# Optimization experiments

Measured on AMD Instinct MI355X. Metric: run time of the kernel, lower is better.

The kernel has to match this reference:

```python
import jax, jax.numpy as jnp
import numpy as np

INP, OUP, KSIZE, STRIDE = 256, 256, 3, 1
M, G = 2, 2
INP_GAP = max(16, INP // 16)  # 16
PAD = KSIZE // 2


def setup_inputs() -> dict:
    key = jax.random.key(0)
    k1, k2, k3, k4, k5 = jax.random.split(key, 5)
    B, H, W = 32, 28, 28
    x = jax.random.normal(k1, (B, INP, H, W), dtype=jnp.float32)
    x_gap = jax.random.normal(k2, (B, INP_GAP, 1, 1), dtype=jnp.float32)
    # wn_fc1: Conv2d(INP_GAP, M*OUP, 1, bias=True) -> dense [M*OUP, INP_GAP]
    w1 = jax.random.normal(k3, (M * OUP, INP_GAP), dtype=jnp.float32) * 0.1
    b1 = jax.random.normal(k4, (M * OUP,), dtype=jnp.float32) * 0.1
    # wn_fc2: grouped 1x1 conv, groups = G*OUP, 1 in-channel per group
    # -> weight is effectively a vector of length OUP*INP*KSIZE*KSIZE
    w2 = jax.random.normal(k5, (OUP * INP * KSIZE * KSIZE,), dtype=jnp.float32) * 0.05
    return {"x": x, "x_gap": x_gap, "w1": w1, "b1": b1, "w2": w2}


def reference(x, x_gap, w1, b1, w2):
    B, _, H, W = x.shape
    # fc1 (1x1 conv on [B, INP_GAP, 1, 1]) + sigmoid -> [B, M*OUP]
    h = jax.nn.sigmoid(jnp.einsum('bi,oi->bo', x_gap[:, :, 0, 0], w1) + b1)
    # fc2: groups = G*OUP, one input channel per group, INP*K*K/G outputs per group
    per = INP * KSIZE * KSIZE // G
    # [B, G*OUP, per] -> per-sample kernels [B*OUP, INP, K, K]
    wk = (w2.reshape(G * OUP, per) * h[:, :, None]).reshape(B * OUP, INP, KSIZE, KSIZE)
    # batched dynamic conv via feature_group_count = B
    y = jax.lax.conv_general_dilated(
        x.reshape(1, B * INP, H, W), wk,
        window_strides=(STRIDE, STRIDE),
        padding=[(PAD, PAD), (PAD, PAD)],
        dimension_numbers=('NCHW', 'OIHW', 'NCHW'),
        feature_group_count=B)
    return y.reshape(B, OUP, y.shape[2], y.shape[3])
```

## Files before the change

### kernel.cpp

```cpp
#include <hip/hip_runtime.h>
#include <hip/hip_bf16.h>

typedef __attribute__((ext_vector_type(8))) short bf16x8;
typedef __attribute__((ext_vector_type(4))) short bf16x4;
typedef __attribute__((ext_vector_type(4))) float f32x4;

#define NB 32
#define NO 256

static __device__ __forceinline__ void gld16(const void* g, void* l) {
    __builtin_amdgcn_global_load_lds(
        (const __attribute__((address_space(1))) void*)g,
        (__attribute__((address_space(3))) void*)l, 16, 0, 0);
}

__global__ void prep_kernel(const float* __restrict__ w2, __hip_bfloat16* __restrict__ wrt) {
    int idx = blockIdx.x * 256 + threadIdx.x;
    int kcol = idx & 15;
    int klo = (idx >> 4) & 3;
    int mf = (idx >> 6) & 3;
    int mw = (idx >> 8) & 3;
    int kw2 = (idx >> 10) & 1;
    int s = idx >> 11;
    int tap = s >> 2;
    int ic = s & 3;
    int o = mw * 64 + mf * 16 + kcol;
    int ch = kw2 * 128 + ic * 32 + klo * 8;
    const float* src = w2 + (size_t)o * 2304 + (size_t)ch * 9 + tap;
    union { bf16x8 v; __hip_bfloat16 e[8]; } u;
#pragma unroll
    for (int e = 0; e < 8; ++e) u.e[e] = __float2bfloat16(src[e * 9]);
    *(bf16x8*)((short*)wrt + (size_t)idx * 8) = u.v;
}

#define MM(A_, B_, mf_, nf_) \
    acc[mf_][nf_] = __builtin_amdgcn_mfma_f32_16x16x32_bf16(A_, B_, acc[mf_][nf_], 0, 0, 0);

#define CL_H1(A0, A1, A2, A3, B0, B1, B2, B3)                           \
    __builtin_amdgcn_s_setprio(1);                                      \
    MM(A0, B0, 0, 0) MM(A1, B0, 1, 0) MM(A2, B0, 2, 0) MM(A3, B0, 3, 0) \
    MM(A0, B1, 0, 1) MM(A1, B1, 1, 1) MM(A2, B1, 2, 1) MM(A3, B1, 3, 1) \
    MM(A0, B2, 0, 2) MM(A1, B2, 1, 2) MM(A2, B2, 2, 2) MM(A3, B2, 3, 2) \
    MM(A0, B3, 0, 3) MM(A1, B3, 1, 3) MM(A2, B3, 2, 3) MM(A3, B3, 3, 3) \
    __builtin_amdgcn_s_setprio(0);
#define CL_H2(A0, A1, A2, A3, B4, B5, B6)                               \
    __builtin_amdgcn_s_setprio(1);                                      \
    MM(A0, B4, 0, 4) MM(A1, B4, 1, 4) MM(A2, B4, 2, 4) MM(A3, B4, 3, 4) \
    MM(A0, B5, 0, 5) MM(A1, B5, 1, 5) MM(A2, B5, 2, 5) MM(A3, B5, 3, 5) \
    MM(A0, B6, 0, 6) MM(A1, B6, 1, 6) MM(A2, B6, 2, 6) MM(A3, B6, 3, 6) \
    __builtin_amdgcn_s_setprio(0);

#define LOADB(D0, D1, D2, D3, D4, D5, D6, XO)                                  \
    D0 = *(const bf16x8*)(Xs + ((u[0] ^ ((kk[0] & 7u) << 4)) ^ (XO)));         \
    D1 = *(const bf16x8*)(Xs + ((u[1] ^ ((kk[1] & 7u) << 4)) ^ (XO)));         \
    D2 = *(const bf16x8*)(Xs + ((u[2] ^ ((kk[2] & 7u) << 4)) ^ (XO)));         \
    D3 = *(const bf16x8*)(Xs + ((u[3] ^ ((kk[3] & 7u) << 4)) ^ (XO)));         \
    D4 = *(const bf16x8*)(Xs + ((u[4] ^ ((kk[4] & 7u) << 4)) ^ (XO)));         \
    D5 = *(const bf16x8*)(Xs + ((u[5] ^ ((kk[5] & 7u) << 4)) ^ (XO)));         \
    D6 = *(const bf16x8*)(Xs + ((u[6] ^ ((kk[6] & 7u) << 4)) ^ (XO)));

#define PHASE_E(BUFOFF, XON)                                                  \
    {                                                                         \
        CL_H1(aA0, aA1, aA2, aA3, bA0, bA1, bA2, bA3)                         \
        asm volatile("s_waitcnt vmcnt(4)" ::: "memory");                      \
        aB0 = *(const bf16x8*)(AbR + (BUFOFF));                               \
        aB1 = *(const bf16x8*)(AbR + (BUFOFF) + 1024);                        \
        aB2 = *(const bf16x8*)(AbR + (BUFOFF) + 2048);                        \
        aB3 = *(const bf16x8*)(AbR + (BUFOFF) + 3072);                        \
        gld16(pG, AbW + (BUFOFF));                                            \
        gld16(pG + 1024, AbW + (BUFOFF) + 1024);                              \
        gld16(pG + 2048, AbW + (BUFOFF) + 2048);                              \
        gld16(pG + 3072, AbW + (BUFOFF) + 3072);                              \
        pG += 32768;                                                          \
        LOADB(bB0, bB1, bB2, bB3, bB4, bB5, bB6, XON)                         \
        __builtin_amdgcn_sched_barrier(0);                                    \
        CL_H2(aA0, aA1, aA2, aA3, bA4, bA5, bA6)                              \
    }
#define PHASE_O(BUFOFF, XON)                                                  \
    {                                                                         \
        CL_H1(aB0, aB1, aB2, aB3, bB0, bB1, bB2, bB3)                         \
        asm volatile("s_waitcnt vmcnt(4)" ::: "memory");                      \
        aA0 = *(const bf16x8*)(AbR + (BUFOFF));                               \
        aA1 = *(const bf16x8*)(AbR + (BUFOFF) + 1024);                        \
        aA2 = *(const bf16x8*)(AbR + (BUFOFF) + 2048);                        \
        aA3 = *(const bf16x8*)(AbR + (BUFOFF) + 3072);                        \
        gld16(pG, AbW + (BUFOFF));                                            \
        gld16(pG + 1024, AbW + (BUFOFF) + 1024);                              \
        gld16(pG + 2048, AbW + (BUFOFF) + 2048);                              \
        gld16(pG + 3072, AbW + (BUFOFF) + 3072);                              \
        pG += 32768;                                                          \
        LOADB(bA0, bA1, bA2, bA3, bA4, bA5, bA6, XON)                         \
        __builtin_amdgcn_sched_barrier(0);                                    \
        CL_H2(aB0, aB1, aB2, aB3, bB4, bB5, bB6)                              \
    }

__global__ __launch_bounds__(512, 2) void conv_kernel(
    const float* __restrict__ x, const __hip_bfloat16* __restrict__ wrt,
    const float* __restrict__ xg, const float* __restrict__ w1,
    const float* __restrict__ b1, float* __restrict__ out) {
    __shared__ __align__(16) char SMEM[159744];
    char* Xs = SMEM;
    char* Ab = SMEM + 92160;
    float* hsm = (float*)(SMEM + 157696);
    float* Xf = (float*)SMEM;
    const int bid = blockIdx.x;
    const int v = (bid & 7) * 28 + (bid >> 3);
    const int b = v / 7;
    const int nt = v - b * 7;
    const int tid = threadIdx.x;
    const int lane = tid & 63;
    const int wv = tid >> 6;
    const int mw = wv & 3;
    const int kw2 = wv >> 2;
    const int kcol = lane & 15;
    const int klo = lane >> 4;

    const char* wrtc = (const char*)wrt;
    char* AbW = Ab + wv * 8192;
    const char* AbR = Ab + wv * 8192 + lane * 16;
    const char* pG = wrtc + wv * 4096 + lane * 16;

    gld16(pG, AbW);
    gld16(pG + 1024, AbW + 1024);
    gld16(pG + 2048, AbW + 2048);
    gld16(pG + 3072, AbW + 3072);
    pG += 32768;
    gld16(pG, AbW + 4096);
    gld16(pG + 1024, AbW + 4096 + 1024);
    gld16(pG + 2048, AbW + 4096 + 2048);
    gld16(pG + 3072, AbW + 4096 + 3072);
    pG += 32768;

    {
        float s = b1[tid];
        const float* g = xg + b * 16;
        const float* w = w1 + tid * 16;
#pragma unroll
        for (int c = 0; c < 16; ++c) s += g[c] * w[c];
        hsm[tid] = 1.0f / (1.0f + expf(-s));
    }

    {
        const bf16x8 z = (bf16x8){0, 0, 0, 0, 0, 0, 0, 0};
        for (int e = tid; e < 6 * 2 * 32; e += 512) {
            int w = e & 31;
            int t2 = e >> 5;
            int row = t2 >> 1;
            int col = (t2 & 1) ? 29 : 0;
            *(bf16x8*)(Xs + (row * 30 + col) * 512 + w * 16) = z;
        }
        if (nt == 0) {
            for (int e = tid; e < 30 * 32; e += 512)
                *(bf16x8*)(Xs + (e >> 5) * 512 + (e & 31) * 16) = z;
        }
        if (nt == 6) {
            for (int e = tid; e < 30 * 32; e += 512)
                *(bf16x8*)(Xs + (150 + (e >> 5)) * 512 + (e & 31) * 16) = z;
        }
        const int p0 = nt * 4 - 1;
        const float* xb = x + (size_t)b * 256 * 784;
        for (int c = tid; c < 2688; c += 512) {
            int c4 = c % 7;
            int t2 = c / 7;
            int chq = t2 & 63;
            int row = t2 >> 6;
            int p = p0 + row;
            if (p >= 0 && p < 28) {
                const float* s0 = xb + ((size_t)(chq * 4) * 28 + p) * 28 + 4 * c4;
                f32x4 v0 = *(const f32x4*)(s0);
                f32x4 v1 = *(const f32x4*)(s0 + 784);
                f32x4 v2 = *(const f32x4*)(s0 + 1568);
                f32x4 v3 = *(const f32x4*)(s0 + 2352);
                int w = chq >> 1;
                int qoff = (chq & 1) * 8;
                int spb = row * 30 + 4 * c4 + 1;
#pragma unroll
                for (int k = 0; k < 4; ++k) {
                    int key = (4 * c4 + 1 + k + 4 * row) & 7;
                    union { bf16x4 vv; __hip_bfloat16 e[4]; } pk;
                    pk.e[0] = __float2bfloat16(v0[k]);
                    pk.e[1] = __float2bfloat16(v1[k]);
                    pk.e[2] = __float2bfloat16(v2[k]);
                    pk.e[3] = __float2bfloat16(v3[k]);
                    *(bf16x4*)(Xs + (spb + k) * 512 + (((w ^ key) << 4) | qoff)) = pk.vv;
                }
            }
        }
    }
    __syncthreads();

    unsigned u[7], kk[7];
#pragma unroll
    for (int nf = 0; nf < 7; ++nf) {
        int n = nf * 16 + kcol;
        int r0 = n / 28;
        int q0 = n - r0 * 28;
        u[nf] = (unsigned)((r0 * 30 + q0) * 512 + (klo << 4));
        kk[nf] = (unsigned)(q0 + 4 * r0);
    }
    const unsigned xo0 = (unsigned)((kw2 * 4 + 0) << 6);
    const unsigned xo1 = (unsigned)((kw2 * 4 + 1) << 6);
    const unsigned xo2 = (unsigned)((kw2 * 4 + 2) << 6);
    const unsigned xo3 = (unsigned)((kw2 * 4 + 3) << 6);

    f32x4 acc[4][7];
#pragma unroll
    for (int mf = 0; mf < 4; ++mf)
#pragma unroll
        for (int nf = 0; nf < 7; ++nf) acc[mf][nf] = (f32x4){0.f, 0.f, 0.f, 0.f};

    bf16x8 aA0, aA1, aA2, aA3, aB0, aB1, aB2, aB3;
    bf16x8 bA0, bA1, bA2, bA3, bA4, bA5, bA6;
    bf16x8 bB0, bB1, bB2, bB3, bB4, bB5, bB6;

    aA0 = *(const bf16x8*)(AbR);
    aA1 = *(const bf16x8*)(AbR + 1024);
    aA2 = *(const bf16x8*)(AbR + 2048);
    aA3 = *(const bf16x8*)(AbR + 3072);
    gld16(pG, AbW);
    gld16(pG + 1024, AbW + 1024);
    gld16(pG + 2048, AbW + 2048);
    gld16(pG + 3072, AbW + 3072);
    pG += 32768;
    LOADB(bA0, bA1, bA2, bA3, bA4, bA5, bA6, xo0)

    for (int tap = 0; tap < 9; ++tap) {
        PHASE_E(4096, xo1)
        PHASE_O(0, xo2)
        PHASE_E(4096, xo3)
        if (tap < 8) {
            const int cross = (tap == 2 || tap == 5);
            const unsigned da = cross ? 28u * 512u : 512u;
            const unsigned dk = cross ? 2u : 1u;
#pragma unroll
            for (int nf = 0; nf < 7; ++nf) { u[nf] += da; kk[nf] += dk; }
        }
        PHASE_O(0, xo0)
    }

    __syncthreads();
    if (kw2 == 1) {
#pragma unroll
        for (int mf = 0; mf < 4; ++mf)
#pragma unroll
            for (int nf = 0; nf < 7; ++nf)
#pragma unroll
                for (int rr = 0; rr < 4; ++rr) {
                    int o = mw * 64 + mf * 16 + klo * 4 + rr;
                    int idx = (((mw * 4 + mf) * 7 + nf) * 4 + rr) * 64 + lane;
                    Xf[idx] = hsm[2 * o + 1] * acc[mf][nf][rr];
                }
    }
    __syncthreads();
    if (kw2 == 0) {
#pragma unroll
        for (int mf = 0; mf < 4; ++mf)
#pragma unroll
            for (int nf = 0; nf < 7; ++nf)
#pragma unroll
                for (int rr = 0; rr < 4; ++rr) {
                    int o = mw * 64 + mf * 16 + klo * 4 + rr;
                    int idx = (((mw * 4 + mf) * 7 + nf) * 4 + rr) * 64 + lane;
                    float y = hsm[2 * o] * acc[mf][nf][rr] + Xf[idx];
                    out[((size_t)b * NO + o) * 784 + nt * 112 + nf * 16 + kcol] = y;
                }
    }
}

extern "C" void kernel_launch(void* const* d_in, const int* in_sizes, int n_in,
                              void* d_out, int out_size, void* d_ws, size_t ws_size,
                              hipStream_t stream) {
    const float* x = (const float*)d_in[0];
    const float* xg = (const float*)d_in[1];
    const float* w1 = (const float*)d_in[2];
    const float* b1 = (const float*)d_in[3];
    const float* w2 = (const float*)d_in[4];
    float* out = (float*)d_out;

    char* ws = (char*)d_ws;
    __hip_bfloat16* wrt = (__hip_bfloat16*)ws;

    prep_kernel<<<288, 256, 0, stream>>>(w2, wrt);
    conv_kernel<<<224, 512, 0, stream>>>(x, wrt, xg, w1, b1, out);
}
```

Measured before the change: 44.11 us.

## Split channel halves across blocks and combine with atomic adds

The 512-thread block that held both input-channel halves is split into two 256-thread blocks, one per half. This doubles the grid to 448 blocks and halves LDS use per block, which allows more blocks per CU. The in-block LDS reduction and its two barriers are replaced by float atomic adds into an output zeroed by a memset, one per channel half. In exchange it adds a memset launch, doubles the global write traffic through atomics, and makes the summation order nondeterministic.

```diff
diff --git a/kernel.cpp b/kernel.cpp
--- a/kernel.cpp
+++ b/kernel.cpp
@@ -5,7 +5,6 @@
 typedef __attribute__((ext_vector_type(4))) short bf16x4;
 typedef __attribute__((ext_vector_type(4))) float f32x4;
 
-#define NB 32
 #define NO 256
 
 static __device__ __forceinline__ void gld16(const void* g, void* l) {
@@ -94,31 +93,30 @@
         CL_H2(aB0, aB1, aB2, aB3, bB4, bB5, bB6)                              \
     }
 
-__global__ __launch_bounds__(512, 2) void conv_kernel(
+__global__ __launch_bounds__(256, 2) void conv_kernel(
     const float* __restrict__ x, const __hip_bfloat16* __restrict__ wrt,
     const float* __restrict__ xg, const float* __restrict__ w1,
     const float* __restrict__ b1, float* __restrict__ out) {
-    __shared__ __align__(16) char SMEM[159744];
+    __shared__ __align__(16) char SMEM[79872];
     char* Xs = SMEM;
-    char* Ab = SMEM + 92160;
-    float* hsm = (float*)(SMEM + 157696);
-    float* Xf = (float*)SMEM;
+    char* Ab = SMEM + 46080;
+    float* hsm = (float*)(SMEM + 78848);
     const int bid = blockIdx.x;
-    const int v = (bid & 7) * 28 + (bid >> 3);
-    const int b = v / 7;
-    const int nt = v - b * 7;
+    const int v = (bid & 7) * 56 + (bid >> 3);
+    const int kw2 = v & 1;
+    const int pair = v >> 1;
+    const int b = pair / 7;
+    const int nt = pair - b * 7;
     const int tid = threadIdx.x;
     const int lane = tid & 63;
-    const int wv = tid >> 6;
-    const int mw = wv & 3;
-    const int kw2 = wv >> 2;
+    const int mw = tid >> 6;
     const int kcol = lane & 15;
     const int klo = lane >> 4;
 
     const char* wrtc = (const char*)wrt;
-    char* AbW = Ab + wv * 8192;
-    const char* AbR = Ab + wv * 8192 + lane * 16;
-    const char* pG = wrtc + wv * 4096 + lane * 16;
+    char* AbW = Ab + mw * 8192;
+    const char* AbR = Ab + mw * 8192 + lane * 16;
+    const char* pG = wrtc + (kw2 * 4 + mw) * 4096 + lane * 16;
 
     gld16(pG, AbW);
     gld16(pG + 1024, AbW + 1024);
@@ -132,9 +130,10 @@
     pG += 32768;
 
     {
-        float s = b1[tid];
+        int j = 2 * tid + kw2;
+        float s = b1[j];
         const float* g = xg + b * 16;
-        const float* w = w1 + tid * 16;
+        const float* w = w1 + j * 16;
 #pragma unroll
         for (int c = 0; c < 16; ++c) s += g[c] * w[c];
         hsm[tid] = 1.0f / (1.0f + expf(-s));
@@ -142,28 +141,28 @@
 
     {
         const bf16x8 z = (bf16x8){0, 0, 0, 0, 0, 0, 0, 0};
-        for (int e = tid; e < 6 * 2 * 32; e += 512) {
-            int w = e & 31;
-            int t2 = e >> 5;
+        for (int e = tid; e < 6 * 2 * 16; e += 256) {
+            int w = e & 15;
+            int t2 = e >> 4;
             int row = t2 >> 1;
             int col = (t2 & 1) ? 29 : 0;
-            *(bf16x8*)(Xs + (row * 30 + col) * 512 + w * 16) = z;
+            *(bf16x8*)(Xs + (row * 30 + col) * 256 + w * 16) = z;
         }
         if (nt == 0) {
-            for (int e = tid; e < 30 * 32; e += 512)
-                *(bf16x8*)(Xs + (e >> 5) * 512 + (e & 31) * 16) = z;
+            for (int e = tid; e < 30 * 16; e += 256)
+                *(bf16x8*)(Xs + (e >> 4) * 256 + (e & 15) * 16) = z;
         }
         if (nt == 6) {
-            for (int e = tid; e < 30 * 32; e += 512)
-                *(bf16x8*)(Xs + (150 + (e >> 5)) * 512 + (e & 31) * 16) = z;
+            for (int e = tid; e < 30 * 16; e += 256)
+                *(bf16x8*)(Xs + (150 + (e >> 4)) * 256 + (e & 15) * 16) = z;
         }
         const int p0 = nt * 4 - 1;
-        const float* xb = x + (size_t)b * 256 * 784;
-        for (int c = tid; c < 2688; c += 512) {
+        const float* xb = x + (size_t)b * 256 * 784 + (size_t)kw2 * 128 * 784;
+        for (int c = tid; c < 1344; c += 256) {
             int c4 = c % 7;
             int t2 = c / 7;
-            int chq = t2 & 63;
-            int row = t2 >> 6;
+            int chq = t2 & 31;
+            int row = t2 >> 5;
             int p = p0 + row;
             if (p >= 0 && p < 28) {
                 const float* s0 = xb + ((size_t)(chq * 4) * 28 + p) * 28 + 4 * c4;
@@ -182,7 +181,7 @@
                     pk.e[1] = __float2bfloat16(v1[k]);
                     pk.e[2] = __float2bfloat16(v2[k]);
                     pk.e[3] = __float2bfloat16(v3[k]);
-                    *(bf16x4*)(Xs + (spb + k) * 512 + (((w ^ key) << 4) | qoff)) = pk.vv;
+                    *(bf16x4*)(Xs + (spb + k) * 256 + (((w ^ key) << 4) | qoff)) = pk.vv;
                 }
             }
         }
@@ -195,13 +194,13 @@
         int n = nf * 16 + kcol;
         int r0 = n / 28;
         int q0 = n - r0 * 28;
-        u[nf] = (unsigned)((r0 * 30 + q0) * 512 + (klo << 4));
+        u[nf] = (unsigned)((r0 * 30 + q0) * 256 + (klo << 4));
         kk[nf] = (unsigned)(q0 + 4 * r0);
     }
-    const unsigned xo0 = (unsigned)((kw2 * 4 + 0) << 6);
-    const unsigned xo1 = (unsigned)((kw2 * 4 + 1) << 6);
-    const unsigned xo2 = (unsigned)((kw2 * 4 + 2) << 6);
-    const unsigned xo3 = (unsigned)((kw2 * 4 + 3) << 6);
+    const unsigned xo0 = 0u << 6;
+    const unsigned xo1 = 1u << 6;
+    const unsigned xo2 = 2u << 6;
+    const unsigned xo3 = 3u << 6;
 
     f32x4 acc[4][7];
 #pragma unroll
@@ -230,7 +229,7 @@
         PHASE_E(4096, xo3)
         if (tap < 8) {
             const int cross = (tap == 2 || tap == 5);
-            const unsigned da = cross ? 28u * 512u : 512u;
+            const unsigned da = cross ? 28u * 256u : 256u;
             const unsigned dk = cross ? 2u : 1u;
 #pragma unroll
             for (int nf = 0; nf < 7; ++nf) { u[nf] += da; kk[nf] += dk; }
@@ -238,32 +237,18 @@
         PHASE_O(0, xo0)
     }
 
-    __syncthreads();
-    if (kw2 == 1) {
-#pragma unroll
-        for (int mf = 0; mf < 4; ++mf)
-#pragma unroll
-            for (int nf = 0; nf < 7; ++nf)
-#pragma unroll
-                for (int rr = 0; rr < 4; ++rr) {
-                    int o = mw * 64 + mf * 16 + klo * 4 + rr;
-                    int idx = (((mw * 4 + mf) * 7 + nf) * 4 + rr) * 64 + lane;
-                    Xf[idx] = hsm[2 * o + 1] * acc[mf][nf][rr];
-                }
-    }
-    __syncthreads();
-    if (kw2 == 0) {
-#pragma unroll
-        for (int mf = 0; mf < 4; ++mf)
-#pragma unroll
-            for (int nf = 0; nf < 7; ++nf)
-#pragma unroll
-                for (int rr = 0; rr < 4; ++rr) {
-                    int o = mw * 64 + mf * 16 + klo * 4 + rr;
-                    int idx = (((mw * 4 + mf) * 7 + nf) * 4 + rr) * 64 + lane;
-                    float y = hsm[2 * o] * acc[mf][nf][rr] + Xf[idx];
-                    out[((size_t)b * NO + o) * 784 + nt * 112 + nf * 16 + kcol] = y;
-                }
+#pragma unroll
+    for (int mf = 0; mf < 4; ++mf) {
+#pragma unroll
+        for (int rr = 0; rr < 4; ++rr) {
+            int o = mw * 64 + mf * 16 + klo * 4 + rr;
+            float hv = hsm[o];
+            float* ob = out + ((size_t)b * NO + o) * 784 + nt * 112 + kcol;
+#pragma unroll
+            for (int nf = 0; nf < 7; ++nf) {
+                unsafeAtomicAdd(ob + nf * 16, hv * acc[mf][nf][rr]);
+            }
+        }
     }
 }
 
@@ -281,5 +266,6 @@
     __hip_bfloat16* wrt = (__hip_bfloat16*)ws;
 
     prep_kernel<<<288, 256, 0, stream>>>(w2, wrt);
-    conv_kernel<<<224, 512, 0, stream>>>(x, wrt, xg, w1, b1, out);
-}
+    hipMemsetAsync(out, 0, (size_t)out_size * sizeof(float), stream);
+    conv_kernel<<<448, 256, 0, stream>>>(x, wrt, xg, w1, b1, out);
+}
```

Measured after the change: 76.63 us. +73.7%, slower.

## Load weight fragments directly from global into registers instead of via LDS staging

Applied to the files above, without the earlier changes.

Drops the global_load_lds staging buffer for the A (weight) operand. Each wave now loads its weight fragments straight from global memory into registers, double-buffered across even and odd phases. This removes the LDS round trip and the explicit vmcnt waits, and shrinks shared memory by about 43 KB. In exchange, global latency is hidden only by register prefetch one phase ahead, which raises VGPR pressure, and the extra sched_barriers constrain instruction interleaving.

```diff
diff --git a/kernel.cpp b/kernel.cpp
--- a/kernel.cpp
+++ b/kernel.cpp
@@ -5,14 +5,7 @@
 typedef __attribute__((ext_vector_type(4))) short bf16x4;
 typedef __attribute__((ext_vector_type(4))) float f32x4;
 
-#define NB 32
 #define NO 256
-
-static __device__ __forceinline__ void gld16(const void* g, void* l) {
-    __builtin_amdgcn_global_load_lds(
-        (const __attribute__((address_space(1))) void*)g,
-        (__attribute__((address_space(3))) void*)l, 16, 0, 0);
-}
 
 __global__ void prep_kernel(const float* __restrict__ w2, __hip_bfloat16* __restrict__ wrt) {
     int idx = blockIdx.x * 256 + threadIdx.x;
@@ -59,49 +52,43 @@
     D5 = *(const bf16x8*)(Xs + ((u[5] ^ ((kk[5] & 7u) << 4)) ^ (XO)));         \
     D6 = *(const bf16x8*)(Xs + ((u[6] ^ ((kk[6] & 7u) << 4)) ^ (XO)));
 
-#define PHASE_E(BUFOFF, XON)                                                  \
+#define GLOADA(S0, S1, S2, S3)                   \
+    S0 = *(const bf16x8*)(pA);                   \
+    S1 = *(const bf16x8*)(pA + 1024);            \
+    S2 = *(const bf16x8*)(pA + 2048);            \
+    S3 = *(const bf16x8*)(pA + 3072);            \
+    pA += 32768;
+
+#define PHASE_E(XON)                                                          \
     {                                                                         \
-        CL_H1(aA0, aA1, aA2, aA3, bA0, bA1, bA2, bA3)                         \
-        asm volatile("s_waitcnt vmcnt(4)" ::: "memory");                      \
-        aB0 = *(const bf16x8*)(AbR + (BUFOFF));                               \
-        aB1 = *(const bf16x8*)(AbR + (BUFOFF) + 1024);                        \
-        aB2 = *(const bf16x8*)(AbR + (BUFOFF) + 2048);                        \
-        aB3 = *(const bf16x8*)(AbR + (BUFOFF) + 3072);                        \
-        gld16(pG, AbW + (BUFOFF));                                            \
-        gld16(pG + 1024, AbW + (BUFOFF) + 1024);                              \
-        gld16(pG + 2048, AbW + (BUFOFF) + 2048);                              \
-        gld16(pG + 3072, AbW + (BUFOFF) + 3072);                              \
-        pG += 32768;                                                          \
-        LOADB(bB0, bB1, bB2, bB3, bB4, bB5, bB6, XON)                         \
-        __builtin_amdgcn_sched_barrier(0);                                    \
-        CL_H2(aA0, aA1, aA2, aA3, bA4, bA5, bA6)                              \
-    }
-#define PHASE_O(BUFOFF, XON)                                                  \
+        CL_H1(aE0, aE1, aE2, aE3, bc0, bc1, bc2, bc3)                         \
+        __builtin_amdgcn_sched_barrier(0);                                    \
+        LOADB(bn0, bn1, bn2, bn3, bn4, bn5, bn6, XON)                         \
+        __builtin_amdgcn_sched_barrier(0);                                    \
+        CL_H2(aE0, aE1, aE2, aE3, bc4, bc5, bc6)                              \
+        __builtin_amdgcn_sched_barrier(0);                                    \
+        GLOADA(aE0, aE1, aE2, aE3)                                            \
+        __builtin_amdgcn_sched_barrier(0);                                    \
+    }
+#define PHASE_O(XON)                                                          \
     {                                                                         \
-        CL_H1(aB0, aB1, aB2, aB3, bB0, bB1, bB2, bB3)                         \
-        asm volatile("s_waitcnt vmcnt(4)" ::: "memory");                      \
-        aA0 = *(const bf16x8*)(AbR + (BUFOFF));                               \
-        aA1 = *(const bf16x8*)(AbR + (BUFOFF) + 1024);                        \
-        aA2 = *(const bf16x8*)(AbR + (BUFOFF) + 2048);                        \
-        aA3 = *(const bf16x8*)(AbR + (BUFOFF) + 3072);                        \
-        gld16(pG, AbW + (BUFOFF));                                            \
-        gld16(pG + 1024, AbW + (BUFOFF) + 1024);                              \
-        gld16(pG + 2048, AbW + (BUFOFF) + 2048);                              \
-        gld16(pG + 3072, AbW + (BUFOFF) + 3072);                              \
-        pG += 32768;                                                          \
-        LOADB(bA0, bA1, bA2, bA3, bA4, bA5, bA6, XON)                         \
-        __builtin_amdgcn_sched_barrier(0);                                    \
-        CL_H2(aB0, aB1, aB2, aB3, bB4, bB5, bB6)                              \
+        CL_H1(aO0, aO1, aO2, aO3, bn0, bn1, bn2, bn3)                         \
+        __builtin_amdgcn_sched_barrier(0);                                    \
+        LOADB(bc0, bc1, bc2, bc3, bc4, bc5, bc6, XON)                         \
+        __builtin_amdgcn_sched_barrier(0);                                    \
+        CL_H2(aO0, aO1, aO2, aO3, bn4, bn5, bn6)                              \
+        __builtin_amdgcn_sched_barrier(0);                                    \
+        GLOADA(aO0, aO1, aO2, aO3)                                            \
+        __builtin_amdgcn_sched_barrier(0);                                    \
     }
 
 __global__ __launch_bounds__(512, 2) void conv_kernel(
     const float* __restrict__ x, const __hip_bfloat16* __restrict__ wrt,
     const float* __restrict__ xg, const float* __restrict__ w1,
     const float* __restrict__ b1, float* __restrict__ out) {
-    __shared__ __align__(16) char SMEM[159744];
+    __shared__ __align__(16) char SMEM[116736];
     char* Xs = SMEM;
-    char* Ab = SMEM + 92160;
-    float* hsm = (float*)(SMEM + 157696);
+    float* hsm = (float*)(SMEM + 114688);
     float* Xf = (float*)SMEM;
     const int bid = blockIdx.x;
     const int v = (bid & 7) * 28 + (bid >> 3);
@@ -115,21 +102,7 @@
     const int kcol = lane & 15;
     const int klo = lane >> 4;
 
-    const char* wrtc = (const char*)wrt;
-    char* AbW = Ab + wv * 8192;
-    const char* AbR = Ab + wv * 8192 + lane * 16;
-    const char* pG = wrtc + wv * 4096 + lane * 16;
-
-    gld16(pG, AbW);
-    gld16(pG + 1024, AbW + 1024);
-    gld16(pG + 2048, AbW + 2048);
-    gld16(pG + 3072, AbW + 3072);
-    pG += 32768;
-    gld16(pG, AbW + 4096);
-    gld16(pG + 1024, AbW + 4096 + 1024);
-    gld16(pG + 2048, AbW + 4096 + 2048);
-    gld16(pG + 3072, AbW + 4096 + 3072);
-    pG += 32768;
+    const char* pA = (const char*)wrt + (kw2 * 4 + mw) * 4096 + lane * 16;
 
     {
         float s = b1[tid];
@@ -209,25 +182,18 @@
 #pragma unroll
         for (int nf = 0; nf < 7; ++nf) acc[mf][nf] = (f32x4){0.f, 0.f, 0.f, 0.f};
 
-    bf16x8 aA0, aA1, aA2, aA3, aB0, aB1, aB2, aB3;
-    bf16x8 bA0, bA1, bA2, bA3, bA4, bA5, bA6;
-    bf16x8 bB0, bB1, bB2, bB3, bB4, bB5, bB6;
-
-    aA0 = *(const bf16x8*)(AbR);
-    aA1 = *(const bf16x8*)(AbR + 1024);
-    aA2 = *(const bf16x8*)(AbR + 2048);
-    aA3 = *(const bf16x8*)(AbR + 3072);
-    gld16(pG, AbW);
-    gld16(pG + 1024, AbW + 1024);
-    gld16(pG + 2048, AbW + 2048);
-    gld16(pG + 3072, AbW + 3072);
-    pG += 32768;
-    LOADB(bA0, bA1, bA2, bA3, bA4, bA5, bA6, xo0)
+    bf16x8 aE0, aE1, aE2, aE3, aO0, aO1, aO2, aO3;
+    bf16x8 bc0, bc1, bc2, bc3, bc4, bc5, bc6;
+    bf16x8 bn0, bn1, bn2, bn3, bn4, bn5, bn6;
+
+    GLOADA(aE0, aE1, aE2, aE3)
+    GLOADA(aO0, aO1, aO2, aO3)
+    LOADB(bc0, bc1, bc2, bc3, bc4, bc5, bc6, xo0)
 
     for (int tap = 0; tap < 9; ++tap) {
-        PHASE_E(4096, xo1)
-        PHASE_O(0, xo2)
-        PHASE_E(4096, xo3)
+        PHASE_E(xo1)
+        PHASE_O(xo2)
+        PHASE_E(xo3)
         if (tap < 8) {
             const int cross = (tap == 2 || tap == 5);
             const unsigned da = cross ? 28u * 512u : 512u;
@@ -235,7 +201,7 @@
 #pragma unroll
             for (int nf = 0; nf < 7; ++nf) { u[nf] += da; kk[nf] += dk; }
         }
-        PHASE_O(0, xo0)
+        PHASE_O(xo0)
     }
 
     __syncthreads();
```

New measurement: 42.07 us. -4.6%, faster.
